# Kernel tuning notes

Hardware: AMD Instinct MI355X
Metric: run time of the kernel (lower is better)

Reference implementation:

```python
import jax, jax.numpy as jnp
import numpy as np

B, L, D, H = 4, 1024, 1024, 16
HD = D // H  # head_dim = 64
SCALE = HD ** -0.5


def setup_inputs() -> dict:
    key = jax.random.key(0)
    k1, k2, k3, k4 = jax.random.split(key, 4)
    x = jax.random.normal(k1, (B, L, D), dtype=jnp.float32)
    # torch nn.Linear(dim, 3*dim): y = x @ W.T + b; we store W already transposed to [D, 3D]
    Wqkv = jax.random.normal(k2, (D, 3 * D), dtype=jnp.float32) * (D ** -0.5)
    bqkv = jax.random.normal(k3, (3 * D,), dtype=jnp.float32) * 0.02
    # distance_embedding: nn.Embedding(2*length - 1, head_dim)
    dist_emb = jax.random.normal(k4, (2 * L - 1, HD), dtype=jnp.float32) * 0.02
    return {"x": x, "Wqkv": Wqkv, "bqkv": bqkv, "dist_emb": dist_emb}


def reference(x, Wqkv, bqkv, dist_emb):
    b, l, d = x.shape
    # QKV projection -> [3, B, H, L, HD]
    qkv = (x @ Wqkv + bqkv).reshape(b, l, 3, H, HD).transpose(2, 0, 3, 1, 4)
    q, k, v = qkv[0], qkv[1], qkv[2]
    # raw attention scores: [B, H, L, L]
    scores = jnp.einsum("bhld,bhmd->bhlm", q, k)
    # relative position bias (relative_key_query branch)
    pos = jnp.arange(l)
    distance = pos[:, None] - pos[None, :]          # [L, L] in [-(L-1), L-1]
    pe = dist_emb[distance + (L - 1)]               # [L, L, HD]
    rel_q = jnp.einsum("bhld,lrd->bhlr", q, pe)
    rel_k = jnp.einsum("bhrd,lrd->bhlr", k, pe)
    scores = (scores + rel_q + rel_k) * SCALE
    probs = jax.nn.softmax(scores, axis=-1)
    out = jnp.einsum("bhlm,bhmd->bhld", probs, v)   # [B, H, L, HD]
    return out.transpose(0, 2, 1, 3).reshape(b, l, d)
```

## Files before the change

### kernel.cpp

```cpp
#include <hip/hip_runtime.h>
#include <hip/hip_bf16.h>
#include <math.h>

#define Bq 4
#define Lq 1024
#define Dq 1024
#define Hq 16
#define HDq 64
#define BHq (Bq * Hq)
#define HEAD_ELEMS ((size_t)BHq * Lq * HDq)

typedef short bf16x8 __attribute__((ext_vector_type(8)));
typedef _Float16 f16x8 __attribute__((ext_vector_type(8)));
typedef float f32x4 __attribute__((ext_vector_type(4)));
#define MFMA16B(A, B, C) __builtin_amdgcn_mfma_f32_16x16x32_bf16(A, B, C, 0, 0, 0)
#define MFMA16F(A, B, C) __builtin_amdgcn_mfma_f32_16x16x32_f16(A, B, C, 0, 0, 0)

#if __has_builtin(__builtin_amdgcn_exp2f)
#define EXP2F(x) __builtin_amdgcn_exp2f(x)
#else
#define EXP2F(x) __expf((x) * 0.6931471805599453f)
#endif

__device__ __forceinline__ unsigned short f2bf(float x) {
  unsigned u = __builtin_bit_cast(unsigned, x);
  unsigned r = u + 0x7FFFu + ((u >> 16) & 1u);
  return (unsigned short)(r >> 16);
}
__device__ __forceinline__ float bf2f(unsigned short s) {
  unsigned u = ((unsigned)s) << 16;
  return __builtin_bit_cast(float, u);
}
__device__ __forceinline__ unsigned short f2h(float x) {
  _Float16 h = (_Float16)x;
  return __builtin_bit_cast(unsigned short, h);
}

__global__ __launch_bounds__(256) void x_prep(const float* __restrict__ X,
                                              unsigned short* __restrict__ Xh) {
  size_t i = (size_t)blockIdx.x * 256 + threadIdx.x;
  float4 f = *(const float4*)(X + i * 4);
  uint2 pk;
  pk.x = (unsigned)f2h(f.x) | ((unsigned)f2h(f.y) << 16);
  pk.y = (unsigned)f2h(f.z) | ((unsigned)f2h(f.w) << 16);
  *(uint2*)(Xh + i * 4) = pk;
}

__global__ __launch_bounds__(256) void wt_prep(const float* __restrict__ W,
                                               unsigned short* __restrict__ Wt) {
  __shared__ unsigned short tile[64 * 72];
  const int k0 = blockIdx.x * 64;
  const int n0 = blockIdx.y * 64;
  const int tid = threadIdx.x;
#pragma unroll
  for (int it = 0; it < 4; it++) {
    int idx = tid + it * 256;
    int r = idx >> 4, c4 = (idx & 15) * 4;
    float4 f = *(const float4*)(W + (size_t)(k0 + r) * 3072 + n0 + c4);
    unsigned w0 = (unsigned)f2h(f.x) | ((unsigned)f2h(f.y) << 16);
    unsigned w1 = (unsigned)f2h(f.z) | ((unsigned)f2h(f.w) << 16);
    *(unsigned*)&tile[r * 72 + c4] = w0;
    *(unsigned*)&tile[r * 72 + c4 + 2] = w1;
  }
  __syncthreads();
#pragma unroll
  for (int it = 0; it < 4; it++) {
    int u = tid + it * 256;
    int n = u >> 4, k4 = (u & 15) * 4;
    unsigned short e0 = tile[(k4 + 0) * 72 + n];
    unsigned short e1 = tile[(k4 + 1) * 72 + n];
    unsigned short e2 = tile[(k4 + 2) * 72 + n];
    unsigned short e3 = tile[(k4 + 3) * 72 + n];
    uint2 pk;
    pk.x = (unsigned)e0 | ((unsigned)e1 << 16);
    pk.y = (unsigned)e2 | ((unsigned)e3 << 16);
    *(uint2*)(Wt + (size_t)(n0 + n) * 1024 + k0 + k4) = pk;
  }
}

__global__ __launch_bounds__(256) void emb_prep(const float* __restrict__ e,
                                                unsigned short* __restrict__ o) {
  int i = blockIdx.x * 256 + threadIdx.x;
  if (i < 2047 * 64) {
    int row = i >> 6, c = i & 63;
    o[(row << 6) | (c ^ ((row & 7) << 3))] = f2bf(e[i]);
  }
}

__global__ __launch_bounds__(256, 2) void qkv_mfma(
    const unsigned short* __restrict__ Xh, const unsigned short* __restrict__ Wt,
    const float* __restrict__ bias, unsigned short* __restrict__ qkvg) {
  __shared__ __align__(16) char smem[32768];
  unsigned short* Asm = (unsigned short*)smem;
  unsigned short* Bsm = (unsigned short*)(smem + 8192);
  unsigned short* Cs  = (unsigned short*)smem;

  const int tid = threadIdx.x;
  const int w = tid >> 6, lane = tid & 63;
  const int col = lane & 15, quad = lane >> 4;
  const int wm = (w >> 1) * 64, wn = (w & 1) * 64;
  const int bn = blockIdx.x * 128, bm = blockIdx.y * 128;

  const unsigned short* Ag = Xh + (size_t)bm * 1024;
  const unsigned short* Bg = Wt + (size_t)bn * 1024;
  const int ldrow = w * 32 + (lane >> 2);
  const int ldoff = (lane & 3) * 8;

  f32x4 acc[4][4];
#pragma unroll
  for (int i = 0; i < 4; i++)
#pragma unroll
    for (int j = 0; j < 4; j++) acc[i][j] = (f32x4){0.f, 0.f, 0.f, 0.f};

  for (int k0 = 0; k0 < 1024; k0 += 32) {
    __syncthreads();
#pragma unroll
    for (int it = 0; it < 2; it++) {
      const unsigned short* ga = Ag + (size_t)(ldrow + it * 16) * 1024 + k0 + ldoff;
      const unsigned short* gb = Bg + (size_t)(ldrow + it * 16) * 1024 + k0 + ldoff;
      __builtin_amdgcn_global_load_lds(
          (const __attribute__((address_space(1))) unsigned*)ga,
          (__attribute__((address_space(3))) unsigned*)(Asm + (w * 32 + it * 16) * 32),
          16, 0, 0);
      __builtin_amdgcn_global_load_lds(
          (const __attribute__((address_space(1))) unsigned*)gb,
          (__attribute__((address_space(3))) unsigned*)(Bsm + (w * 32 + it * 16) * 32),
          16, 0, 0);
    }
    __syncthreads();
    f16x8 af[4], bf[4];
#pragma unroll
    for (int i = 0; i < 4; i++)
      af[i] = *(const f16x8*)&Asm[(wm + i * 16 + col) * 32 + quad * 8];
#pragma unroll
    for (int j = 0; j < 4; j++)
      bf[j] = *(const f16x8*)&Bsm[(wn + j * 16 + col) * 32 + quad * 8];
#pragma unroll
    for (int i = 0; i < 4; i++)
#pragma unroll
      for (int j = 0; j < 4; j++)
        acc[i][j] = MFMA16F(af[i], bf[j], acc[i][j]);
  }

  float bj[4];
#pragma unroll
  for (int j = 0; j < 4; j++) bj[j] = bias[bn + wn + j * 16 + col];

  __syncthreads();
#pragma unroll
  for (int i = 0; i < 4; i++)
#pragma unroll
    for (int j = 0; j < 4; j++)
#pragma unroll
      for (int k = 0; k < 4; k++)
        Cs[(wm + i * 16 + quad * 4 + k) * 128 + wn + j * 16 + col] =
            f2bf(acc[i][j][k] + bj[j]);
  __syncthreads();

  const int t = bn >> 10;
  unsigned short* dst_base = qkvg + (size_t)t * HEAD_ELEMS;
#pragma unroll
  for (int it = 0; it < 8; it++) {
    int u = tid + it * 256;
    int row = u >> 4, c8 = (u & 15) * 8;
    int m = bm + row;
    int n = bn + c8;
    int b = m >> 10, l = m & 1023;
    int cc = n & 1023, h = cc >> 6, d0 = cc & 63;
    if (t != 2) d0 ^= ((l & 7) << 3);
    uint4 val = *(const uint4*)&Cs[row * 128 + c8];
    *(uint4*)(dst_base + (((size_t)(b * 16 + h) * 1024 + l) * 64 + d0)) = val;
  }
}

__global__ __launch_bounds__(256) void vt_prep_bf(const unsigned short* __restrict__ vg,
                                                  unsigned short* __restrict__ vtg) {
  __shared__ unsigned short tile[64 * 72];
  const int bh = blockIdx.x;
  const int rt = blockIdx.y * 64;
  const int tid = threadIdx.x;
  const unsigned short* src = vg + ((size_t)bh * Lq + rt) * HDq;
#pragma unroll
  for (int it = 0; it < 2; it++) {
    int idx = tid + it * 256;
    int r = idx >> 3, o = (idx & 7) * 8;
    *(uint4*)&tile[r * 72 + o] = *(const uint4*)(src + (size_t)r * 64 + o);
  }
  __syncthreads();
  unsigned short* dst = vtg + (size_t)bh * HDq * Lq;
#pragma unroll
  for (int it = 0; it < 4; it++) {
    int u = tid + it * 256;
    int d = u >> 4, r4 = (u & 15) * 4;
    unsigned short e0 = tile[(r4 + 0) * 72 + d];
    unsigned short e1 = tile[(r4 + 1) * 72 + d];
    unsigned short e2 = tile[(r4 + 2) * 72 + d];
    unsigned short e3 = tile[(r4 + 3) * 72 + d];
    uint2 pk;
    pk.x = (unsigned)e0 | ((unsigned)e1 << 16);
    pk.y = (unsigned)e2 | ((unsigned)e3 << 16);
    int r4s = r4 ^ ((d & 7) << 3);
    *(uint2*)(dst + (size_t)d * Lq + rt + r4s) = pk;
  }
}

__global__ __launch_bounds__(256, 2) void attn_mfma(
    const unsigned short* __restrict__ qg, const unsigned short* __restrict__ kg,
    const unsigned short* __restrict__ vtg, const unsigned short* __restrict__ emb,
    float* __restrict__ out) {
  __shared__ __align__(16) char smem[50176];
  unsigned short* Ps  = (unsigned short*)smem;
  unsigned short* Ks  = (unsigned short*)(smem + 8192);
  unsigned short* VTs = (unsigned short*)(smem + 16384);
  unsigned short* Pb  = (unsigned short*)(smem + 24576);
  unsigned short* B12 = (unsigned short*)(smem + 32768);

  const int bh = blockIdx.x;
  const int l0 = blockIdx.y * 64;
  const int tid = threadIdx.x;
  const int w = tid >> 6, lane = tid & 63;
  const int col = lane & 15, quad = lane >> 4;
  const int lw = w * 16;
  const int fo = quad * 8;
  const int swm = (col & 7) << 3;

  const unsigned short* Qg = qg + ((size_t)bh * Lq + l0) * HDq;
  const unsigned short* Kp = kg + (size_t)bh * Lq * HDq;
  const unsigned short* Vp = vtg + (size_t)bh * HDq * Lq;

  bf16x8 qf[2];
#pragma unroll
  for (int ks = 0; ks < 2; ks++)
    qf[ks] = *(const bf16x8*)(Qg + (size_t)(lw + col) * 64 + ((fo + ks * 32) ^ swm));

  bf16x8 sav[4][2];
#pragma unroll
  for (int dm = 0; dm < 4; dm++) {
    int g = l0 + 1024 + dm * 16 + col;
    g = (g > 2046) ? 2046 : g;
    int m = (g & 7) << 3;
#pragma unroll
    for (int ks = 0; ks < 2; ks++)
      sav[dm][ks] = *(const bf16x8*)(emb + (size_t)g * 64 + ((fo + ks * 32) ^ m));
  }

  f32x4 oacc[4];
#pragma unroll
  for (int nt = 0; nt < 4; nt++) oacc[nt] = (f32x4){0.f, 0.f, 0.f, 0.f};
  float mrow[4] = {-1e30f, -1e30f, -1e30f, -1e30f};
  float lrow[4] = {0.f, 0.f, 0.f, 0.f};

  int pb0 = l0 + 960;
  const int lr8 = (lane & 7) * 8;

  for (int ch = 0; ch < 16; ch++) {
    __syncthreads();

#pragma unroll
    for (int it = 0; it < 2; it++) {
      const int rb = w * 16 + it * 8;
      const int r = rb + (lane >> 3);
      __builtin_amdgcn_global_load_lds(
          (const __attribute__((address_space(1))) unsigned*)(Kp + (size_t)r * 64 + lr8),
          (__attribute__((address_space(3))) unsigned*)(Ks + rb * 64), 16, 0, 0);
      __builtin_amdgcn_global_load_lds(
          (const __attribute__((address_space(1))) unsigned*)(Vp + (size_t)r * Lq + lr8),
          (__attribute__((address_space(3))) unsigned*)(VTs + rb * 64), 16, 0, 0);
      __builtin_amdgcn_global_load_lds(
          (const __attribute__((address_space(1))) unsigned*)(emb + (size_t)(pb0 + r) * 64 + lr8),
          (__attribute__((address_space(3))) unsigned*)(Pb + rb * 64), 16, 0, 0);
    }
    __syncthreads();

    bf16x8 kf[4][2];
#pragma unroll
    for (int rt = 0; rt < 4; rt++)
#pragma unroll
      for (int ks = 0; ks < 2; ks++)
        kf[rt][ks] = *(const bf16x8*)&Ks[((rt * 16 + col) << 6) + ((fo + ks * 32) ^ swm)];
    f32x4 sac[4];
#pragma unroll
    for (int rt = 0; rt < 4; rt++) {
      f32x4 z = (f32x4){0.f, 0.f, 0.f, 0.f};
      z = MFMA16B(qf[0], kf[rt][0], z);
      z = MFMA16B(qf[1], kf[rt][1], z);
      sac[rt] = z;
    }

    bf16x8 kaf[2];
#pragma unroll
    for (int ks = 0; ks < 2; ks++)
      kaf[ks] = *(const bf16x8*)&Ks[((lw + col) << 6) + ((fo + ks * 32) ^ swm)];

    bf16x8 fresh[4][2];
#pragma unroll
    for (int dm = 0; dm < 4; dm++)
#pragma unroll
      for (int ks = 0; ks < 2; ks++)
        fresh[dm][ks] = *(const bf16x8*)&Pb[((dm * 16 + col) << 6) + ((fo + ks * 32) ^ swm)];

#pragma unroll
    for (int dt = 0; dt < 8; dt++) {
      bf16x8 pbf0 = (dt < 4) ? fresh[dt & 3][0] : sav[dt & 3][0];
      bf16x8 pbf1 = (dt < 4) ? fresh[dt & 3][1] : sav[dt & 3][1];
      f32x4 z = (f32x4){0.f, 0.f, 0.f, 0.f};
      f32x4 y = (f32x4){0.f, 0.f, 0.f, 0.f};
      z = MFMA16B(qf[0], pbf0, z);
      z = MFMA16B(qf[1], pbf1, z);
      y = MFMA16B(kaf[0], pbf0, y);
      y = MFMA16B(kaf[1], pbf1, y);
      const int dcol = dt * 16 + col;
#pragma unroll
      for (int k = 0; k < 4; k++) {
        int l1 = lw + quad * 4 + k;
        int r1 = l1 - dcol + 63;
        if (r1 >= 0 && r1 < 64) B12[l1 * 136 + 2 * r1] = f2bf(z[k]);
        int r2 = lw + quad * 4 + k;
        int l2 = dcol - 63 + r2;
        if (l2 >= 0 && l2 < 64) B12[l2 * 136 + 2 * r2 + 1] = f2bf(y[k]);
      }
    }
#pragma unroll
    for (int dm = 0; dm < 4; dm++)
#pragma unroll
      for (int ks = 0; ks < 2; ks++)
        sav[dm][ks] = fresh[dm][ks];
    __syncthreads();

    float p[4][4];
    float alpha[4];
#pragma unroll
    for (int k = 0; k < 4; k++) {
      int l1 = lw + quad * 4 + k;
      float st[4];
#pragma unroll
      for (int rt = 0; rt < 4; rt++) {
        int r = rt * 16 + col;
        unsigned pr = *(const unsigned*)&B12[l1 * 136 + 2 * r];
        float bias = bf2f((unsigned short)(pr & 0xFFFFu)) +
                     bf2f((unsigned short)(pr >> 16));
        st[rt] = (sac[rt][k] + bias) * 0.18033688011112042f;
      }
      float mx = fmaxf(fmaxf(st[0], st[1]), fmaxf(st[2], st[3]));
      mx = fmaxf(mx, __shfl_xor(mx, 1));
      mx = fmaxf(mx, __shfl_xor(mx, 2));
      mx = fmaxf(mx, __shfl_xor(mx, 4));
      mx = fmaxf(mx, __shfl_xor(mx, 8));
      float mnew = fmaxf(mrow[k], mx);
      float a = EXP2F(mrow[k] - mnew);
      mrow[k] = mnew;
      alpha[k] = a;
      float ls = 0.f;
#pragma unroll
      for (int rt = 0; rt < 4; rt++) {
        p[rt][k] = EXP2F(st[rt] - mnew);
        ls += p[rt][k];
      }
      lrow[k] = lrow[k] * a + ls;
    }
#pragma unroll
    for (int nt = 0; nt < 4; nt++)
#pragma unroll
      for (int k = 0; k < 4; k++) oacc[nt][k] *= alpha[k];

#pragma unroll
    for (int rt = 0; rt < 4; rt++)
#pragma unroll
      for (int k = 0; k < 4; k++) {
        int l1 = lw + quad * 4 + k;
        Ps[(l1 << 6) + ((rt * 16 + col) ^ ((l1 & 7) << 3))] = f2bf(p[rt][k]);
      }

    bf16x8 pf[2];
#pragma unroll
    for (int ks = 0; ks < 2; ks++)
      pf[ks] = *(const bf16x8*)&Ps[((lw + col) << 6) + ((fo + ks * 32) ^ swm)];
#pragma unroll
    for (int nt = 0; nt < 4; nt++) {
      bf16x8 v0 = *(const bf16x8*)&VTs[((nt * 16 + col) << 6) + (fo ^ swm)];
      bf16x8 v1 = *(const bf16x8*)&VTs[((nt * 16 + col) << 6) + ((fo + 32) ^ swm)];
      oacc[nt] = MFMA16B(pf[0], v0, oacc[nt]);
      oacc[nt] = MFMA16B(pf[1], v1, oacc[nt]);
    }

    Kp += 64 * 64;
    Vp += 64;
    pb0 -= 64;
  }

  float inv[4];
#pragma unroll
  for (int k = 0; k < 4; k++) {
    float t = lrow[k];
    t += __shfl_xor(t, 1);
    t += __shfl_xor(t, 2);
    t += __shfl_xor(t, 4);
    t += __shfl_xor(t, 8);
    inv[k] = 1.0f / t;
  }
  const int b = bh >> 4, h = bh & 15;
#pragma unroll
  for (int nt = 0; nt < 4; nt++) {
#pragma unroll
    for (int k = 0; k < 4; k++) {
      int lg = l0 + lw + quad * 4 + k;
      int d = nt * 16 + col;
      out[(((size_t)b * Lq + lg) * Hq + h) * HDq + d] = oacc[nt][k] * inv[k];
    }
  }
}

extern "C" void kernel_launch(void* const* d_in, const int* in_sizes, int n_in,
                              void* d_out, int out_size, void* d_ws, size_t ws_size,
                              hipStream_t stream) {
  const float* x        = (const float*)d_in[0];
  const float* Wqkv     = (const float*)d_in[1];
  const float* bqkv     = (const float*)d_in[2];
  const float* dist_emb = (const float*)d_in[3];
  float* out = (float*)d_out;

  unsigned short* Xh   = (unsigned short*)d_ws;
  unsigned short* Wt   = (unsigned short*)((char*)d_ws + (8u << 20));
  unsigned short* qkvg = (unsigned short*)((char*)d_ws + (16u << 20));
  unsigned short* vtg  = (unsigned short*)((char*)d_ws + (40u << 20));
  unsigned short* emb  = (unsigned short*)((char*)d_ws + (48u << 20));

  x_prep<<<dim3(4096), dim3(256), 0, stream>>>(x, Xh);
  wt_prep<<<dim3(16, 48), dim3(256), 0, stream>>>(Wqkv, Wt);
  emb_prep<<<dim3(512), dim3(256), 0, stream>>>(dist_emb, emb);

  qkv_mfma<<<dim3(24, 32), dim3(256), 0, stream>>>(Xh, Wt, bqkv, qkvg);

  vt_prep_bf<<<dim3(BHq, Lq / 64), dim3(256), 0, stream>>>(qkvg + 2 * HEAD_ELEMS, vtg);

  attn_mfma<<<dim3(BHq, Lq / 64), dim3(256), 0, stream>>>(
      qkvg, qkvg + HEAD_ELEMS, vtg, emb, out);
}
```

Baseline: 257.1 us.

## Merge prep kernels, fuse V transpose into QKV epilogue, alias attention LDS

```diff
diff --git a/kernel.cpp b/kernel.cpp
--- a/kernel.cpp
+++ b/kernel.cpp
@@ -36,60 +36,61 @@
   return __builtin_bit_cast(unsigned short, h);
 }
 
-__global__ __launch_bounds__(256) void x_prep(const float* __restrict__ X,
-                                              unsigned short* __restrict__ Xh) {
-  size_t i = (size_t)blockIdx.x * 256 + threadIdx.x;
-  float4 f = *(const float4*)(X + i * 4);
-  uint2 pk;
-  pk.x = (unsigned)f2h(f.x) | ((unsigned)f2h(f.y) << 16);
-  pk.y = (unsigned)f2h(f.z) | ((unsigned)f2h(f.w) << 16);
-  *(uint2*)(Xh + i * 4) = pk;
-}
-
-__global__ __launch_bounds__(256) void wt_prep(const float* __restrict__ W,
-                                               unsigned short* __restrict__ Wt) {
+__global__ __launch_bounds__(256) void prep_all(
+    const float* __restrict__ X, unsigned short* __restrict__ Xh,
+    const float* __restrict__ W, unsigned short* __restrict__ Wt,
+    const float* __restrict__ e, unsigned short* __restrict__ o) {
   __shared__ unsigned short tile[64 * 72];
-  const int k0 = blockIdx.x * 64;
-  const int n0 = blockIdx.y * 64;
+  const int bid = blockIdx.x;
   const int tid = threadIdx.x;
-#pragma unroll
-  for (int it = 0; it < 4; it++) {
-    int idx = tid + it * 256;
-    int r = idx >> 4, c4 = (idx & 15) * 4;
-    float4 f = *(const float4*)(W + (size_t)(k0 + r) * 3072 + n0 + c4);
-    unsigned w0 = (unsigned)f2h(f.x) | ((unsigned)f2h(f.y) << 16);
-    unsigned w1 = (unsigned)f2h(f.z) | ((unsigned)f2h(f.w) << 16);
-    *(unsigned*)&tile[r * 72 + c4] = w0;
-    *(unsigned*)&tile[r * 72 + c4 + 2] = w1;
-  }
-  __syncthreads();
-#pragma unroll
-  for (int it = 0; it < 4; it++) {
-    int u = tid + it * 256;
-    int n = u >> 4, k4 = (u & 15) * 4;
-    unsigned short e0 = tile[(k4 + 0) * 72 + n];
-    unsigned short e1 = tile[(k4 + 1) * 72 + n];
-    unsigned short e2 = tile[(k4 + 2) * 72 + n];
-    unsigned short e3 = tile[(k4 + 3) * 72 + n];
+  if (bid < 4096) {
+    size_t i = (size_t)bid * 256 + tid;
+    float4 f = *(const float4*)(X + i * 4);
     uint2 pk;
-    pk.x = (unsigned)e0 | ((unsigned)e1 << 16);
-    pk.y = (unsigned)e2 | ((unsigned)e3 << 16);
-    *(uint2*)(Wt + (size_t)(n0 + n) * 1024 + k0 + k4) = pk;
-  }
-}
-
-__global__ __launch_bounds__(256) void emb_prep(const float* __restrict__ e,
-                                                unsigned short* __restrict__ o) {
-  int i = blockIdx.x * 256 + threadIdx.x;
-  if (i < 2047 * 64) {
-    int row = i >> 6, c = i & 63;
-    o[(row << 6) | (c ^ ((row & 7) << 3))] = f2bf(e[i]);
+    pk.x = (unsigned)f2h(f.x) | ((unsigned)f2h(f.y) << 16);
+    pk.y = (unsigned)f2h(f.z) | ((unsigned)f2h(f.w) << 16);
+    *(uint2*)(Xh + i * 4) = pk;
+  } else if (bid < 4864) {
+    const int wb = bid - 4096;
+    const int k0 = (wb & 15) * 64;
+    const int n0 = (wb >> 4) * 64;
+#pragma unroll
+    for (int it = 0; it < 4; it++) {
+      int idx = tid + it * 256;
+      int r = idx >> 4, c4 = (idx & 15) * 4;
+      float4 f = *(const float4*)(W + (size_t)(k0 + r) * 3072 + n0 + c4);
+      unsigned w0 = (unsigned)f2h(f.x) | ((unsigned)f2h(f.y) << 16);
+      unsigned w1 = (unsigned)f2h(f.z) | ((unsigned)f2h(f.w) << 16);
+      *(unsigned*)&tile[r * 72 + c4] = w0;
+      *(unsigned*)&tile[r * 72 + c4 + 2] = w1;
+    }
+    __syncthreads();
+#pragma unroll
+    for (int it = 0; it < 4; it++) {
+      int u = tid + it * 256;
+      int n = u >> 4, k4 = (u & 15) * 4;
+      unsigned short e0 = tile[(k4 + 0) * 72 + n];
+      unsigned short e1 = tile[(k4 + 1) * 72 + n];
+      unsigned short e2 = tile[(k4 + 2) * 72 + n];
+      unsigned short e3 = tile[(k4 + 3) * 72 + n];
+      uint2 pk;
+      pk.x = (unsigned)e0 | ((unsigned)e1 << 16);
+      pk.y = (unsigned)e2 | ((unsigned)e3 << 16);
+      *(uint2*)(Wt + (size_t)(n0 + n) * 1024 + k0 + k4) = pk;
+    }
+  } else {
+    int i = (bid - 4864) * 256 + tid;
+    if (i < 2047 * 64) {
+      int row = i >> 6, c = i & 63;
+      o[(row << 6) | (c ^ ((row & 7) << 3))] = f2bf(e[i]);
+    }
   }
 }
 
 __global__ __launch_bounds__(256, 2) void qkv_mfma(
     const unsigned short* __restrict__ Xh, const unsigned short* __restrict__ Wt,
-    const float* __restrict__ bias, unsigned short* __restrict__ qkvg) {
+    const float* __restrict__ bias, unsigned short* __restrict__ qkvg,
+    unsigned short* __restrict__ vtg) {
   __shared__ __align__(16) char smem[32768];
   unsigned short* Asm = (unsigned short*)smem;
   unsigned short* Bsm = (unsigned short*)(smem + 8192);
@@ -152,55 +153,53 @@
 #pragma unroll
     for (int j = 0; j < 4; j++)
 #pragma unroll
-      for (int k = 0; k < 4; k++)
-        Cs[(wm + i * 16 + quad * 4 + k) * 128 + wn + j * 16 + col] =
-            f2bf(acc[i][j][k] + bj[j]);
+      for (int k = 0; k < 4; k++) {
+        int row = wm + i * 16 + quad * 4 + k;
+        int c = wn + j * 16 + col;
+        Cs[row * 128 + (c ^ ((row & 7) << 3))] = f2bf(acc[i][j][k] + bj[j]);
+      }
   __syncthreads();
 
   const int t = bn >> 10;
-  unsigned short* dst_base = qkvg + (size_t)t * HEAD_ELEMS;
-#pragma unroll
-  for (int it = 0; it < 8; it++) {
-    int u = tid + it * 256;
-    int row = u >> 4, c8 = (u & 15) * 8;
-    int m = bm + row;
-    int n = bn + c8;
-    int b = m >> 10, l = m & 1023;
-    int cc = n & 1023, h = cc >> 6, d0 = cc & 63;
-    if (t != 2) d0 ^= ((l & 7) << 3);
-    uint4 val = *(const uint4*)&Cs[row * 128 + c8];
-    *(uint4*)(dst_base + (((size_t)(b * 16 + h) * 1024 + l) * 64 + d0)) = val;
-  }
-}
-
-__global__ __launch_bounds__(256) void vt_prep_bf(const unsigned short* __restrict__ vg,
-                                                  unsigned short* __restrict__ vtg) {
-  __shared__ unsigned short tile[64 * 72];
-  const int bh = blockIdx.x;
-  const int rt = blockIdx.y * 64;
-  const int tid = threadIdx.x;
-  const unsigned short* src = vg + ((size_t)bh * Lq + rt) * HDq;
-#pragma unroll
-  for (int it = 0; it < 2; it++) {
-    int idx = tid + it * 256;
-    int r = idx >> 3, o = (idx & 7) * 8;
-    *(uint4*)&tile[r * 72 + o] = *(const uint4*)(src + (size_t)r * 64 + o);
-  }
-  __syncthreads();
-  unsigned short* dst = vtg + (size_t)bh * HDq * Lq;
-#pragma unroll
-  for (int it = 0; it < 4; it++) {
-    int u = tid + it * 256;
-    int d = u >> 4, r4 = (u & 15) * 4;
-    unsigned short e0 = tile[(r4 + 0) * 72 + d];
-    unsigned short e1 = tile[(r4 + 1) * 72 + d];
-    unsigned short e2 = tile[(r4 + 2) * 72 + d];
-    unsigned short e3 = tile[(r4 + 3) * 72 + d];
-    uint2 pk;
-    pk.x = (unsigned)e0 | ((unsigned)e1 << 16);
-    pk.y = (unsigned)e2 | ((unsigned)e3 << 16);
-    int r4s = r4 ^ ((d & 7) << 3);
-    *(uint2*)(dst + (size_t)d * Lq + rt + r4s) = pk;
+  if (t != 2) {
+    unsigned short* dst_base = qkvg + (size_t)t * HEAD_ELEMS;
+#pragma unroll
+    for (int it = 0; it < 8; it++) {
+      int u = tid + it * 256;
+      int row = u >> 4, c8 = (u & 15) * 8;
+      int m = bm + row;
+      int n = bn + c8;
+      int b = m >> 10, l = m & 1023;
+      int cc = n & 1023, h = cc >> 6;
+      int d0 = (cc & 63) ^ ((l & 7) << 3);
+      uint4 val = *(const uint4*)&Cs[row * 128 + (c8 ^ ((row & 7) << 3))];
+      *(uint4*)(dst_base + (((size_t)(b * 16 + h) * 1024 + l) * 64 + d0)) = val;
+    }
+  } else {
+    const int b = bm >> 10, lblk = bm & 1023;
+    const int h0 = (bn & 1023) >> 6;
+#pragma unroll
+    for (int it = 0; it < 16; it++) {
+      int u = tid + it * 256;
+      int hh = u >> 11;
+      int rem = u & 2047;
+      int cc2 = rem >> 10;
+      int rem2 = rem & 1023;
+      int d = rem2 >> 4;
+      int r4 = (rem2 & 15) * 4;
+      int c = hh * 64 + d;
+      int rb = cc2 * 64 + r4;
+      unsigned short e0 = Cs[(rb + 0) * 128 + (c ^ (((rb + 0) & 7) << 3))];
+      unsigned short e1 = Cs[(rb + 1) * 128 + (c ^ (((rb + 1) & 7) << 3))];
+      unsigned short e2 = Cs[(rb + 2) * 128 + (c ^ (((rb + 2) & 7) << 3))];
+      unsigned short e3 = Cs[(rb + 3) * 128 + (c ^ (((rb + 3) & 7) << 3))];
+      uint2 pk;
+      pk.x = (unsigned)e0 | ((unsigned)e1 << 16);
+      pk.y = (unsigned)e2 | ((unsigned)e3 << 16);
+      int r4s = r4 ^ ((d & 7) << 3);
+      size_t bh = (size_t)(b * 16 + h0 + hh);
+      *(uint2*)(vtg + bh * ((size_t)HDq * Lq) + (size_t)d * Lq + lblk + cc2 * 64 + r4s) = pk;
+    }
   }
 }
 
@@ -208,12 +207,12 @@
     const unsigned short* __restrict__ qg, const unsigned short* __restrict__ kg,
     const unsigned short* __restrict__ vtg, const unsigned short* __restrict__ emb,
     float* __restrict__ out) {
-  __shared__ __align__(16) char smem[50176];
-  unsigned short* Ps  = (unsigned short*)smem;
-  unsigned short* Ks  = (unsigned short*)(smem + 8192);
-  unsigned short* VTs = (unsigned short*)(smem + 16384);
-  unsigned short* Pb  = (unsigned short*)(smem + 24576);
-  unsigned short* B12 = (unsigned short*)(smem + 32768);
+  __shared__ __align__(16) char smem[41984];
+  unsigned short* Ks  = (unsigned short*)smem;
+  unsigned short* VTs = (unsigned short*)(smem + 8192);
+  unsigned short* Pb  = (unsigned short*)(smem + 16384);
+  unsigned short* Ps  = Pb;
+  unsigned short* B12 = (unsigned short*)(smem + 24576);
 
   const int bh = blockIdx.x;
   const int l0 = blockIdx.y * 64;
@@ -425,13 +424,9 @@
   unsigned short* vtg  = (unsigned short*)((char*)d_ws + (40u << 20));
   unsigned short* emb  = (unsigned short*)((char*)d_ws + (48u << 20));
 
-  x_prep<<<dim3(4096), dim3(256), 0, stream>>>(x, Xh);
-  wt_prep<<<dim3(16, 48), dim3(256), 0, stream>>>(Wqkv, Wt);
-  emb_prep<<<dim3(512), dim3(256), 0, stream>>>(dist_emb, emb);
-
-  qkv_mfma<<<dim3(24, 32), dim3(256), 0, stream>>>(Xh, Wt, bqkv, qkvg);
-
-  vt_prep_bf<<<dim3(BHq, Lq / 64), dim3(256), 0, stream>>>(qkvg + 2 * HEAD_ELEMS, vtg);
+  prep_all<<<dim3(5376), dim3(256), 0, stream>>>(x, Xh, Wqkv, Wt, dist_emb, emb);
+
+  qkv_mfma<<<dim3(24, 32), dim3(256), 0, stream>>>(Xh, Wt, bqkv, qkvg, vtg);
 
   attn_mfma<<<dim3(BHq, Lq / 64), dim3(256), 0, stream>>>(
       qkvg, qkvg + HEAD_ELEMS, vtg, emb, out);
```

After: 246.6 us. -4.1%, faster.
